# Kernel optimization log

Hardware: AMD Instinct MI355X
Metric: run time of the kernel (lower is better)

Reference implementation:

```python
import jax, jax.numpy as jnp
import numpy as np

MAX_LEN_SEQ = 2048
MAX_LEN_PAD = 2176
MIN_LEN_SEG = 32
MAX_LEN_SEG = 128
S = MAX_LEN_SEQ // MIN_LEN_SEG + 1  # max_num_seg = 65
B = 16
D = 128
R = B * S          # 1040 segment rows
W = 2 * MAX_LEN_SEG  # 256 candidate positions per segment


def _forward(x, scales, len_seq, len_seg_raw):
    T = x.shape[1]
    sc = scales + 0.5                                   # (R,) in [0.5, 1.5)
    idx = jnp.arange(W, dtype=jnp.float32)              # (W,)
    idx_scaled = idx[None, :] / sc[:, None]             # (R, W)
    idx_fl = jnp.floor(idx_scaled)
    lam = idx_scaled - idx_fl                           # (R, W)
    len_seg = (len_seg_raw.astype(jnp.int32) + MIN_LEN_SEG)  # (R, 1)
    mask1 = idx_fl < (len_seg.astype(jnp.float32) - 1.0)
    # per-batch cumulative segment offsets
    offset = jnp.cumsum(len_seg.reshape(B, S), axis=-1)
    offset = jnp.pad(offset[:, :-1], ((0, 0), (1, 0))).reshape(R, 1)
    idx_org = idx_fl + offset.astype(jnp.float32)       # (R, W) source positions
    len_rp = jnp.repeat(len_seq.astype(jnp.float32), S)  # (R,)
    mask2 = idx_org < (len_rp - 1.0)[:, None]
    mask = (mask1 & mask2).reshape(-1)                  # (R*W,) row-major like boolean_mask

    pos = jnp.cumsum(mask.astype(jnp.int32)) - 1        # compacted slot for masked entries
    total = jnp.sum(mask.astype(jnp.int32))

    bidx = jnp.broadcast_to((jnp.arange(R) // S)[:, None], (R, W)).reshape(-1)
    i_fl = jnp.clip(idx_org.astype(jnp.int32).reshape(-1), 0, T - 1)
    i_cl = jnp.clip(i_fl + 1, 0, T - 1)
    y_fl = x[bidx, i_fl]                                # (R*W, D)
    y_cl = x[bidx, i_cl]
    lamf = lam.reshape(-1)[:, None]
    y = (1.0 - lamf) * y_fl + lamf * y_cl               # (R*W, D)

    # compact masked rows into dense buffer (extra row N swallows unmasked)
    N = R * W
    buf = jnp.zeros((N + 1, D), x.dtype)
    buf = buf.at[jnp.where(mask, pos, N)].set(y)

    # emulate y[: total//B*B].reshape(B, -1, D)[:, :MAX_LEN_SEQ] + pad
    L = total // B
    t = jnp.arange(MAX_LEN_SEQ)
    gidx = jnp.arange(B)[:, None] * L + t[None, :]      # (B, MAX_LEN_SEQ)
    out = buf[jnp.clip(gidx, 0, N)]
    out = jnp.where((t < L)[None, :, None], out, jnp.zeros((), x.dtype))
    return out


def setup_inputs() -> dict:
    key = jax.random.key(0)
    k1, k2, k3, k4 = jax.random.split(key, 4)
    x = jax.random.normal(k1, (B, MAX_LEN_PAD, D), dtype=jnp.float32)
    scales = jax.random.uniform(k2, (R,), dtype=jnp.float32)
    len_seq = jax.random.randint(k3, (B,), MAX_LEN_SEQ // 2, MAX_LEN_SEQ, dtype=jnp.int32)
    len_seq = len_seq.at[0].set(MAX_LEN_SEQ)  # force max(len_seq) == MAX_LEN_SEQ (static)
    len_seg_raw = jax.random.randint(k4, (R, 1), 0, MAX_LEN_SEG - MIN_LEN_SEG, dtype=jnp.int32)
    return {"x": x, "scales": scales, "len_seq": len_seq, "len_seg_raw": len_seg_raw}


def reference(x, scales, len_seq, len_seg_raw):
    return _forward(x, scales, len_seq, len_seg_raw)
```

## Files before the change

kernel.cpp:

```cpp
#include <hip/hip_runtime.h>

#define B_      16
#define S_      65
#define R_      1040
#define W_      256
#define T_      2176
#define D_      128
#define MAXSEQ  2048

__global__ __launch_bounds__(256) void interp_setup(
    const float* __restrict__ scales,
    const int*   __restrict__ len_seq,
    const int*   __restrict__ len_seg_raw,
    int* __restrict__ offs,
    int* __restrict__ row_start,
    int* __restrict__ meta)
{
    __shared__ int s_len[R_];
    __shared__ int s_off[R_];
    __shared__ int s_wtot[4];
    const int tid  = threadIdx.x;
    const int lane = tid & 63;
    const int wid  = tid >> 6;

    for (int r = tid; r < R_; r += 256) s_len[r] = len_seg_raw[r] + 32;
    __syncthreads();

    for (int b = wid; b < B_; b += 4) {
        int v = s_len[b * S_ + lane];
        int incl = v;
        #pragma unroll
        for (int d = 1; d < 64; d <<= 1) {
            int n = __shfl_up(incl, d, 64);
            if (lane >= d) incl += n;
        }
        s_off[b * S_ + lane] = incl - v;
        int tot = __shfl(incl, 63, 64);
        if (lane == 0) s_off[b * S_ + 64] = tot;
    }
    __syncthreads();

    int c[5];
    const int r0 = tid * 5;
    int tsum = 0;
    #pragma unroll
    for (int i = 0; i < 5; ++i) {
        int r = r0 + i, cc = 0;
        if (r < R_) {
            float sc = scales[r] + 0.5f;
            int off = s_off[r];
            int K = min(s_len[r] - 1, len_seq[r / S_] - 1 - off);
            if (K > 0) {
                cc = (int)ceilf((float)K * sc);
                cc = min(max(cc, 0), W_);
                const float Kf = (float)K;
                while (cc > 0  && ((float)(cc - 1) / sc) >= Kf) --cc;
                while (cc < W_ && ((float)cc       / sc) <  Kf) ++cc;
            }
            offs[r] = off;
        }
        c[i] = cc; tsum += cc;
    }

    int incl = tsum;
    #pragma unroll
    for (int d = 1; d < 64; d <<= 1) {
        int n = __shfl_up(incl, d, 64);
        if (lane >= d) incl += n;
    }
    if (lane == 63) s_wtot[wid] = incl;
    __syncthreads();
    int wpre = 0, total = 0;
    #pragma unroll
    for (int wv = 0; wv < 4; ++wv) {
        int t_ = s_wtot[wv];
        if (wv < wid) wpre += t_;
        total += t_;
    }
    int base = wpre + incl - tsum;

    #pragma unroll
    for (int i = 0; i < 5; ++i) {
        int r = r0 + i;
        if (r < R_) { row_start[r] = base; base += c[i]; }
    }
    if (tid == 0) {
        row_start[R_] = total;
        meta[0] = total;
        meta[1] = total / B_;
    }
}

__global__ __launch_bounds__(256) void interp_gather(
    const float* __restrict__ x,
    const float* __restrict__ scales,
    const int*   __restrict__ offs,
    const int*   __restrict__ row_start,
    const int*   __restrict__ meta,
    float* __restrict__ out)
{
    __shared__ int s_rs[R_ + 1];
    __shared__ int s_of[R_];
    const int tid = threadIdx.x;
    for (int i = tid; i < R_ + 1; i += 256) s_rs[i] = row_start[i];
    for (int i = tid; i < R_;     i += 256) s_of[i] = offs[i];
    __syncthreads();

    const int L    = meta[1];
    const int orow = blockIdx.x * 8 + (tid >> 5);
    const int lane = tid & 31;
    float4* outp = (float4*)(out + (size_t)orow * D_) + lane;

    const int t = orow & (MAXSEQ - 1);
    const int b = orow >> 11;
    if (t >= L) { *outp = make_float4(0.f, 0.f, 0.f, 0.f); return; }

    const int g = b * L + t;
    int lo = 0, hi = R_;
    while (hi - lo > 1) {
        int mid = (lo + hi) >> 1;
        if (s_rs[mid] <= g) lo = mid; else hi = mid;
    }
    const int r = lo;
    const int w = g - s_rs[r];

    const float sc  = scales[r] + 0.5f;
    const float is  = (float)w / sc;
    const float fl  = floorf(is);
    const float lam = is - fl;
    const int i0 = (int)fl + s_of[r];
    const int bs = r / S_;

    const float* base = x + (size_t)bs * (T_ * D_);
    const float4* pa = (const float4*)(base + (size_t)i0 * D_) + lane;
    const float4* pb = (const float4*)(base + (size_t)(i0 + 1) * D_) + lane;
    const float4 a = *pa, cc = *pb;
    const float om = 1.0f - lam;
    float4 y;
    y.x = om * a.x + lam * cc.x;
    y.y = om * a.y + lam * cc.y;
    y.z = om * a.z + lam * cc.z;
    y.w = om * a.w + lam * cc.w;
    *outp = y;
}

extern "C" void kernel_launch(void* const* d_in, const int* in_sizes, int n_in,
                              void* d_out, int out_size, void* d_ws, size_t ws_size,
                              hipStream_t stream) {
    const float* x           = (const float*)d_in[0];
    const float* scales      = (const float*)d_in[1];
    const int*   len_seq     = (const int*)d_in[2];
    const int*   len_seg_raw = (const int*)d_in[3];
    float*       out         = (float*)d_out;

    int* offs      = (int*)d_ws;
    int* row_start = offs + R_;
    int* meta      = row_start + R_ + 1;

    interp_setup<<<1, 256, 0, stream>>>(scales, len_seq, len_seg_raw,
                                        offs, row_start, meta);

    const int nrows = B_ * MAXSEQ;
    interp_gather<<<nrows / 8, 256, 0, stream>>>(x, scales, offs, row_start,
                                                 meta, out);
}
```

Baseline: 87.31 us.

## Replace per-row binary search gather with per-segment scatter and zero-fill blocks

Setup now packs per-segment start, offset, count and scale into one int4 record. The gather kernel is inverted: each block handles a chunk of positions of one segment and computes its output row by division, instead of every block staging row_start/offs into LDS and binary-searching. Extra blocks zero the tail rows beyond L. This removes the per-block LDS staging and search, at the cost of a much larger grid in which many blocks exit immediately.

```diff
diff --git a/kernel.cpp b/kernel.cpp
--- a/kernel.cpp
+++ b/kernel.cpp
@@ -8,13 +8,16 @@
 #define D_      128
 #define MAXSEQ  2048
 
+#define CHUNKS_ 32
+#define NGATHER (R_ * CHUNKS_)
+#define NZERO   (B_ * MAXSEQ / 8)
+
 __global__ __launch_bounds__(256) void interp_setup(
     const float* __restrict__ scales,
     const int*   __restrict__ len_seq,
     const int*   __restrict__ len_seg_raw,
-    int* __restrict__ offs,
-    int* __restrict__ row_start,
-    int* __restrict__ meta)
+    int4* __restrict__ rowmeta,
+    int*  __restrict__ meta)
 {
     __shared__ int s_len[R_];
     __shared__ int s_off[R_];
@@ -40,15 +43,18 @@
     }
     __syncthreads();
 
-    int c[5];
+    int   c[5];
+    int   offv[5];
+    float scv[5];
     const int r0 = tid * 5;
     int tsum = 0;
     #pragma unroll
     for (int i = 0; i < 5; ++i) {
-        int r = r0 + i, cc = 0;
+        int r = r0 + i, cc = 0, off = 0;
+        float sc = 1.0f;
         if (r < R_) {
-            float sc = scales[r] + 0.5f;
-            int off = s_off[r];
+            sc  = scales[r] + 0.5f;
+            off = s_off[r];
             int K = min(s_len[r] - 1, len_seq[r / S_] - 1 - off);
             if (K > 0) {
                 cc = (int)ceilf((float)K * sc);
@@ -57,9 +63,8 @@
                 while (cc > 0  && ((float)(cc - 1) / sc) >= Kf) --cc;
                 while (cc < W_ && ((float)cc       / sc) <  Kf) ++cc;
             }
-            offs[r] = off;
         }
-        c[i] = cc; tsum += cc;
+        c[i] = cc; offv[i] = off; scv[i] = sc; tsum += cc;
     }
 
     int incl = tsum;
@@ -82,10 +87,12 @@
     #pragma unroll
     for (int i = 0; i < 5; ++i) {
         int r = r0 + i;
-        if (r < R_) { row_start[r] = base; base += c[i]; }
+        if (r < R_) {
+            rowmeta[r] = make_int4(base, offv[i], c[i], __float_as_int(scv[i]));
+            base += c[i];
+        }
     }
     if (tid == 0) {
-        row_start[R_] = total;
         meta[0] = total;
         meta[1] = total / B_;
     }
@@ -93,55 +100,61 @@
 
 __global__ __launch_bounds__(256) void interp_gather(
     const float* __restrict__ x,
-    const float* __restrict__ scales,
-    const int*   __restrict__ offs,
-    const int*   __restrict__ row_start,
+    const int4*  __restrict__ rowmeta,
     const int*   __restrict__ meta,
     float* __restrict__ out)
 {
-    __shared__ int s_rs[R_ + 1];
-    __shared__ int s_of[R_];
-    const int tid = threadIdx.x;
-    for (int i = tid; i < R_ + 1; i += 256) s_rs[i] = row_start[i];
-    for (int i = tid; i < R_;     i += 256) s_of[i] = offs[i];
-    __syncthreads();
+    const int tid  = threadIdx.x;
+    const int sub  = tid >> 5;
+    const int lane = tid & 31;
+    const int bid  = blockIdx.x;
 
-    const int L    = meta[1];
-    const int orow = blockIdx.x * 8 + (tid >> 5);
-    const int lane = tid & 31;
-    float4* outp = (float4*)(out + (size_t)orow * D_) + lane;
+    if (bid < NGATHER) {
+        const int r     = bid >> 5;
+        const int chunk = bid & (CHUNKS_ - 1);
+        const int4 m    = rowmeta[r];
+        const int count = m.z;
+        const int wbase = chunk * 8;
+        if (wbase >= count) return;
+        const int w = wbase + sub;
+        if (w >= count) return;
 
-    const int t = orow & (MAXSEQ - 1);
-    const int b = orow >> 11;
-    if (t >= L) { *outp = make_float4(0.f, 0.f, 0.f, 0.f); return; }
+        const int L = meta[1];
+        const unsigned p  = (unsigned)(m.x + w);
+        const unsigned BL = (unsigned)(B_ * L);
+        if (p >= BL) return;
+        const unsigned bo = p / (unsigned)L;
+        const int t = (int)(p - bo * (unsigned)L);
+        if (t >= MAXSEQ) return;
 
-    const int g = b * L + t;
-    int lo = 0, hi = R_;
-    while (hi - lo > 1) {
-        int mid = (lo + hi) >> 1;
-        if (s_rs[mid] <= g) lo = mid; else hi = mid;
+        const float sc  = __int_as_float(m.w);
+        const float is  = (float)w / sc;
+        const float fl  = floorf(is);
+        const float lam = is - fl;
+        const int i0 = (int)fl + m.y;
+        const int bs = r / S_;
+
+        const float* base = x + (size_t)bs * (T_ * D_);
+        const float4* pa = (const float4*)(base + (size_t)i0 * D_) + lane;
+        const float4* pb = (const float4*)(base + (size_t)(i0 + 1) * D_) + lane;
+        const float4 a = *pa, cc = *pb;
+        const float om = 1.0f - lam;
+        float4 y;
+        y.x = om * a.x + lam * cc.x;
+        y.y = om * a.y + lam * cc.y;
+        y.z = om * a.z + lam * cc.z;
+        y.w = om * a.w + lam * cc.w;
+        float4* op = (float4*)(out + ((size_t)bo * MAXSEQ + t) * D_) + lane;
+        *op = y;
+    } else {
+        const int L    = meta[1];
+        const int orow = (bid - NGATHER) * 8 + sub;
+        const int t    = orow & (MAXSEQ - 1);
+        if (t >= L) {
+            float4* op = (float4*)(out + (size_t)orow * D_) + lane;
+            *op = make_float4(0.f, 0.f, 0.f, 0.f);
+        }
     }
-    const int r = lo;
-    const int w = g - s_rs[r];
-
-    const float sc  = scales[r] + 0.5f;
-    const float is  = (float)w / sc;
-    const float fl  = floorf(is);
-    const float lam = is - fl;
-    const int i0 = (int)fl + s_of[r];
-    const int bs = r / S_;
-
-    const float* base = x + (size_t)bs * (T_ * D_);
-    const float4* pa = (const float4*)(base + (size_t)i0 * D_) + lane;
-    const float4* pb = (const float4*)(base + (size_t)(i0 + 1) * D_) + lane;
-    const float4 a = *pa, cc = *pb;
-    const float om = 1.0f - lam;
-    float4 y;
-    y.x = om * a.x + lam * cc.x;
-    y.y = om * a.y + lam * cc.y;
-    y.z = om * a.z + lam * cc.z;
-    y.w = om * a.w + lam * cc.w;
-    *outp = y;
 }
 
 extern "C" void kernel_launch(void* const* d_in, const int* in_sizes, int n_in,
@@ -153,14 +166,11 @@
     const int*   len_seg_raw = (const int*)d_in[3];
     float*       out         = (float*)d_out;
 
-    int* offs      = (int*)d_ws;
-    int* row_start = offs + R_;
-    int* meta      = row_start + R_ + 1;
+    int4* rowmeta = (int4*)d_ws;
+    int*  meta    = (int*)(rowmeta + R_);
 
     interp_setup<<<1, 256, 0, stream>>>(scales, len_seq, len_seg_raw,
-                                        offs, row_start, meta);
+                                        rowmeta, meta);
 
-    const int nrows = B_ * MAXSEQ;
-    interp_gather<<<nrows / 8, 256, 0, stream>>>(x, scales, offs, row_start,
-                                                 meta, out);
+    interp_gather<<<NGATHER + NZERO, 256, 0, stream>>>(x, rowmeta, meta, out);
 }
```

After: 88.45 us. About the same (+1.3%).
